# Optimization experiments

Measured on AMD Instinct MI355X. Metric: run time of the kernel, lower is better.

## Reference

```python
import jax, jax.numpy as jnp
import numpy as np

PHI_C = 0.9
ALPHA = 0.9
EPS = 1e-06
K_MAX = 100


def setup_inputs() -> dict:
    key = jax.random.key(0)
    k1, k2, k3 = jax.random.split(key, 3)
    B, D_IN, D_H, D_OUT = 16384, 1024, 4096, 1024
    x = jax.random.normal(k1, (B, D_IN), dtype=jnp.float32)
    W1 = jax.random.normal(k2, (D_IN, D_H), dtype=jnp.float32) * 0.02
    b1 = jnp.zeros((D_H,), dtype=jnp.float32)
    W2 = jax.random.normal(k3, (D_H, D_OUT), dtype=jnp.float32) * 0.02
    b2 = jnp.zeros((D_OUT,), dtype=jnp.float32)
    return {"x": x, "W1": W1, "b1": b1, "W2": W2, "b2": b2}


def _base_net(x, W1, b1, W2, b2):
    h = jax.nn.relu(x @ W1 + b1)
    return h @ W2 + b2  # [B, D_OUT]


def _fixed_point(out):
    # y_{k+1} = y_k + alpha * phi_c * tanh(out - y_k), with early exit when
    # max|y_{k+1} - y_k| < eps (the converging step IS applied, as in torch).
    y0 = jnp.zeros_like(out)

    def step(carry, _):
        y, done = carry
        y_next = y + ALPHA * PHI_C * jnp.tanh(out - y)
        converged = jnp.max(jnp.abs(y_next - y)) < EPS
        y_new = jnp.where(done, y, y_next)
        return (y_new, done | converged), None

    (y, _), _ = jax.lax.scan(step, (y0, jnp.array(False)), None, length=K_MAX)
    return y


def reference(x, W1, b1, W2, b2):
    out = _base_net(x, W1, b1, W2, b2)
    return _fixed_point(out)
```

## Files before the change

### kernel.cpp

```cpp
#include <hip/hip_runtime.h>
#include <hip/hip_bf16.h>
#include <stdint.h>


#define DEV __device__ __forceinline__

typedef short bf16x8 __attribute__((ext_vector_type(8)));
typedef float f32x4 __attribute__((ext_vector_type(4)));

typedef __attribute__((address_space(1))) const unsigned char* gptr1_t;
typedef __attribute__((address_space(3))) unsigned char* lptr3_t;

DEV void async_copy16(const void* g, void* l) {
  __builtin_amdgcn_global_load_lds((gptr1_t)g, (lptr3_t)l, 16, 0, 0);
}

DEV unsigned short f2bf(float f) {
  union { float f; unsigned u; } v; v.f = f;
  unsigned u = v.u + 0x7FFFu + ((v.u >> 16) & 1u);
  return (unsigned short)(u >> 16);
}

#define BAR()  __builtin_amdgcn_s_barrier()
#define VMW(n) asm volatile("s_waitcnt vmcnt(" #n ")" ::: "memory")


__global__ void cvt_f32_bf16(const float4* __restrict__ in,
                             ushort4* __restrict__ out, int n4) {
  int i = blockIdx.x * blockDim.x + threadIdx.x;
  if (i >= n4) return;
  float4 v = in[i];
  ushort4 o;
  o.x = f2bf(v.x); o.y = f2bf(v.y); o.z = f2bf(v.z); o.w = f2bf(v.w);
  out[i] = o;
}

__global__ void transpose_f32_bf16(const float* __restrict__ in,
                                   unsigned short* __restrict__ out,
                                   int R, int C) {
  __shared__ float tile[32][33];
  int c0 = blockIdx.x * 32, r0 = blockIdx.y * 32;
  int tx = threadIdx.x, ty = threadIdx.y;
#pragma unroll
  for (int i = 0; i < 32; i += 8)
    tile[ty + i][tx] = in[(long)(r0 + ty + i) * C + (c0 + tx)];
  __syncthreads();
#pragma unroll
  for (int i = 0; i < 32; i += 8)
    out[(long)(c0 + ty + i) * R + (r0 + tx)] = f2bf(tile[tx][ty + i]);
}


#define LDA(base, m, ks) \
  (*(const bf16x8*)((base) + abase + (m) * 2048 + (c0 ^ ((ks) << 6))))
#define LDB(base, n, ks) \
  (*(const bf16x8*)((base) + bbase + (n) * 2048 + (c0 ^ ((ks) << 6))))

#define RD_A(dst, base, m0_)                                   \
  _Pragma("unroll") for (int m_ = 0; m_ < 4; ++m_) {           \
    dst[m_][0] = LDA(base, (m0_) + m_, 0);                     \
    dst[m_][1] = LDA(base, (m0_) + m_, 1);                     \
  }
#define RD_B(dst, base, n0_)                                   \
  _Pragma("unroll") for (int n_ = 0; n_ < 2; ++n_) {           \
    dst[n_][0] = LDB(base, (n0_) + n_, 0);                     \
    dst[n_][1] = LDB(base, (n0_) + n_, 1);                     \
  }

#define QUAD(MB, NB, AF, BF)                                                \
  do {                                                                      \
    __builtin_amdgcn_s_setprio(1);                                          \
    _Pragma("unroll") for (int m_ = 0; m_ < 4; ++m_)                        \
    _Pragma("unroll") for (int n_ = 0; n_ < 2; ++n_) {                      \
      acc[(MB) + m_][(NB) + n_] = __builtin_amdgcn_mfma_f32_16x16x32_bf16(  \
          AF[m_][0], BF[n_][0], acc[(MB) + m_][(NB) + n_], 0, 0, 0);        \
      acc[(MB) + m_][(NB) + n_] = __builtin_amdgcn_mfma_f32_16x16x32_bf16(  \
          AF[m_][1], BF[n_][1], acc[(MB) + m_][(NB) + n_], 0, 0, 0);        \
    }                                                                       \
    __builtin_amdgcn_s_setprio(0);                                          \
  } while (0)

#define ST_A_LO(dstw, koff) { async_copy16(gA[0] + (koff), (dstw));          \
                              async_copy16(gA[2] + (koff), (dstw) + 16384); }
#define ST_A_HI(dstw, koff) { async_copy16(gA[1] + (koff), (dstw) + 8192);   \
                              async_copy16(gA[3] + (koff), (dstw) + 24576); }
#define ST_B_LO(dstw, koff) { async_copy16(gB[0] + (koff), (dstw));          \
                              async_copy16(gB[1] + (koff), (dstw) + 8192); }
#define ST_B_HI(dstw, koff) { async_copy16(gB[2] + (koff), (dstw) + 16384);  \
                              async_copy16(gB[3] + (koff), (dstw) + 24576); }

template <bool RELU_BF16>
__global__ __launch_bounds__(512, 2)
void gemm256(const unsigned short* __restrict__ A,
             const unsigned short* __restrict__ BT,
             const float* __restrict__ bias,
             void* __restrict__ Cout,
             int M, int N, int K, int nbn_shift) {
  extern __shared__ char lds[];
  const char* aE = lds;
  const char* aO = lds + 32768;
  const char* bE = lds + 65536;
  const char* bO = lds + 98304;

  const int tid = threadIdx.x;
  const int wave = tid >> 6, lane = tid & 63;
  const int wr = wave >> 2, wc = wave & 3;

  char* aEw = (char*)aE + wave * 1024;
  char* aOw = (char*)aO + wave * 1024;
  char* bEw = (char*)bE + wave * 1024;
  char* bOw = (char*)bO + wave * 1024;

  const int nwg = gridDim.x;
  const int wg = blockIdx.x;
  const int swz = (wg & 7) * (nwg >> 3) + (wg >> 3);
  const int bm = swz >> nbn_shift;
  const int bn = swz & ((1 << nbn_shift) - 1);
  const int m0 = bm << 8, n0 = bn << 8;

  const int srow = tid >> 3;
  const int sk = ((tid & 7) ^ (srow & 7)) << 3;
  const unsigned short* gA[4];
  const unsigned short* gB[4];
#pragma unroll
  for (int c = 0; c < 4; ++c) {
    gA[c] = A + (size_t)(m0 + c * 64 + srow) * K + sk;
    gB[c] = BT + (size_t)(n0 + c * 64 + srow) * K + sk;
  }

  const int lr = lane & 15, lg = lane >> 4;
  const int c0 = ((lg ^ (lr & 7)) << 4);
  const int abase = (wr * 128 + lr) * 128;
  const int bbase = (wc * 64 + lr) * 128;

  f32x4 acc[8][4] = {};
  bf16x8 af[4][2], b01[2][2], b23[2][2];

  ST_B_LO(bEw, 0);  ST_B_HI(bEw, 0);
  ST_A_LO(aEw, 0);  ST_A_HI(aEw, 0);
  ST_B_LO(bOw, 64); ST_B_HI(bOw, 64);
  VMW(4);
  BAR();

  const int NT = K >> 6;

  for (int it = 0; it < (NT - 2) / 2; ++it) {
    const int kE = (2 * it) << 6;
    RD_B(b01, bE, 0); RD_A(af, aE, 0); RD_B(b23, bE, 2);
    ST_A_LO(aOw, kE + 64); ST_A_HI(aOw, kE + 64);
    QUAD(0, 0, af, b01); QUAD(0, 2, af, b23);
    BAR();
    RD_A(af, aE, 4);
    ST_B_LO(bEw, kE + 128); ST_B_HI(bEw, kE + 128);
    QUAD(4, 2, af, b23); QUAD(4, 0, af, b01);
    VMW(4); BAR();
    RD_B(b01, bO, 0); RD_A(af, aO, 0); RD_B(b23, bO, 2);
    ST_A_LO(aEw, kE + 128); ST_A_HI(aEw, kE + 128);
    QUAD(0, 0, af, b01); QUAD(0, 2, af, b23);
    BAR();
    RD_A(af, aO, 4);
    ST_B_LO(bOw, kE + 192); ST_B_HI(bOw, kE + 192);
    QUAD(4, 2, af, b23); QUAD(4, 0, af, b01);
    VMW(4); BAR();
  }

  {
    const int kL = (NT - 1) << 6;
    RD_B(b01, bE, 0); RD_A(af, aE, 0); RD_B(b23, bE, 2);
    ST_A_LO(aOw, kL); ST_A_HI(aOw, kL);
    QUAD(0, 0, af, b01); QUAD(0, 2, af, b23);
    BAR();
    RD_A(af, aE, 4);
    QUAD(4, 2, af, b23); QUAD(4, 0, af, b01);
    VMW(0); BAR();
    RD_B(b01, bO, 0); RD_A(af, aO, 0); RD_B(b23, bO, 2);
    QUAD(0, 0, af, b01); QUAD(0, 2, af, b23);
    BAR();
    RD_A(af, aO, 4);
    QUAD(4, 2, af, b23); QUAD(4, 0, af, b01);
  }

  const int ccol = n0 + wc * 64;
  const int crow = m0 + wr * 128;
  float bv[4];
#pragma unroll
  for (int n = 0; n < 4; ++n) bv[n] = bias[ccol + n * 16 + lr];

  if (RELU_BF16) {
    unsigned short* O = (unsigned short*)Cout;
#pragma unroll
    for (int m = 0; m < 8; ++m)
#pragma unroll
      for (int j = 0; j < 4; ++j) {
        size_t r = (size_t)(crow + m * 16 + lg * 4 + j) * N;
#pragma unroll
        for (int n = 0; n < 4; ++n) {
          float v = acc[m][n][j] + bv[n];
          O[r + ccol + n * 16 + lr] = f2bf(fmaxf(v, 0.0f));
        }
      }
  } else {
    float* O = (float*)Cout;
#pragma unroll
    for (int m = 0; m < 8; ++m)
#pragma unroll
      for (int j = 0; j < 4; ++j) {
        size_t r = (size_t)(crow + m * 16 + lg * 4 + j) * N;
#pragma unroll
        for (int n = 0; n < 4; ++n)
          O[r + ccol + n * 16 + lr] = acc[m][n][j] + bv[n];
      }
  }
}


extern "C" void kernel_launch(void* const* d_in, const int* in_sizes, int n_in,
                              void* d_out, int out_size, void* d_ws,
                              size_t ws_size, hipStream_t stream) {
  const float* x  = (const float*)d_in[0];
  const float* W1 = (const float*)d_in[1];
  const float* b1 = (const float*)d_in[2];
  const float* W2 = (const float*)d_in[3];
  const float* b2 = (const float*)d_in[4];
  float* out = (float*)d_out;

  const int B = 16384, DIN = 1024, DH = 4096, DOUT = 1024;

  size_t need = (size_t)B * DIN * 2 + (size_t)DIN * DH * 2 +
                (size_t)DH * DOUT * 2 + (size_t)B * DH * 2;
  if (ws_size < need) return;

  char* ws = (char*)d_ws;
  unsigned short* xb  = (unsigned short*)ws;  ws += (size_t)B * DIN * 2;
  unsigned short* w1t = (unsigned short*)ws;  ws += (size_t)DIN * DH * 2;
  unsigned short* w2t = (unsigned short*)ws;  ws += (size_t)DH * DOUT * 2;
  unsigned short* h   = (unsigned short*)ws;

  hipFuncSetAttribute((const void*)gemm256<true>,
                      hipFuncAttributeMaxDynamicSharedMemorySize, 131072);
  hipFuncSetAttribute((const void*)gemm256<false>,
                      hipFuncAttributeMaxDynamicSharedMemorySize, 131072);

  int n4 = B * DIN / 4;
  cvt_f32_bf16<<<n4 / 256, 256, 0, stream>>>((const float4*)x, (ushort4*)xb, n4);
  transpose_f32_bf16<<<dim3(DH / 32, DIN / 32), dim3(32, 8), 0, stream>>>(W1, w1t, DIN, DH);
  transpose_f32_bf16<<<dim3(DOUT / 32, DH / 32), dim3(32, 8), 0, stream>>>(W2, w2t, DH, DOUT);

  gemm256<true><<<dim3((B / 256) * (DH / 256)), 512, 131072, stream>>>(
      xb, w1t, b1, h, B, DH, DIN, 4);
  gemm256<false><<<dim3((B / 256) * (DOUT / 256)), 512, 131072, stream>>>(
      h, w2t, b2, out, B, DOUT, DH, 2);
}
```

Baseline: 274.5 us.

## Use 4-wave 32x32x16 MFMA GEMM kernel for the first layer

Adds a new GEMM kernel with 256 threads (4 waves), each wave computing a 128x128 tile with 32x32x16 bf16 MFMAs and a double-buffered async global-to-LDS pipeline. It replaces the 8-wave 16x16 kernel for the first (ReLU, bf16 output) GEMM only. The aim is higher per-wave ILP and fewer LDS reads per FLOP. The trade-off is heavy register pressure from 256 accumulator floats per lane and only one workgroup per CU, which may hurt latency hiding.

```diff
diff --git a/kernel.cpp b/kernel.cpp
--- a/kernel.cpp
+++ b/kernel.cpp
@@ -7,6 +7,7 @@
 
 typedef short bf16x8 __attribute__((ext_vector_type(8)));
 typedef float f32x4 __attribute__((ext_vector_type(4)));
+typedef float f32x16 __attribute__((ext_vector_type(16)));
 
 typedef __attribute__((address_space(1))) const unsigned char* gptr1_t;
 typedef __attribute__((address_space(3))) unsigned char* lptr3_t;
@@ -21,8 +22,9 @@
   return (unsigned short)(u >> 16);
 }
 
-#define BAR()  __builtin_amdgcn_s_barrier()
-#define VMW(n) asm volatile("s_waitcnt vmcnt(" #n ")" ::: "memory")
+#define BAR()    __builtin_amdgcn_s_barrier()
+#define VMW(n)   asm volatile("s_waitcnt vmcnt(" #n ")" ::: "memory")
+#define SCHEDB() __builtin_amdgcn_sched_barrier(0)
 
 
 __global__ void cvt_f32_bf16(const float4* __restrict__ in,
@@ -48,6 +50,129 @@
 #pragma unroll
   for (int i = 0; i < 32; i += 8)
     out[(long)(c0 + ty + i) * R + (r0 + tx)] = f2bf(tile[tx][ty + i]);
+}
+
+
+#define ILDA(base, m, ks) \
+  (*(const bf16x8*)((base) + i_abase + (m) * 4096 + (i_c0 ^ ((ks) << 5))))
+#define ILDB(base, n, ks) \
+  (*(const bf16x8*)((base) + i_bbase + (n) * 4096 + (i_c0 ^ ((ks) << 5))))
+
+#define ICOMPUTE(aB, bB)                                                      \
+  _Pragma("unroll") for (int ks = 0; ks < 4; ++ks) {                          \
+    bf16x8 af[4], bfr[4];                                                     \
+    _Pragma("unroll") for (int i = 0; i < 4; ++i) {                           \
+      af[i] = ILDA(aB, i, ks);                                                \
+      bfr[i] = ILDB(bB, i, ks);                                               \
+    }                                                                         \
+    _Pragma("unroll") for (int m_ = 0; m_ < 4; ++m_)                          \
+    _Pragma("unroll") for (int n_ = 0; n_ < 4; ++n_)                          \
+      acc[m_][n_] = __builtin_amdgcn_mfma_f32_32x32x16_bf16(                  \
+          af[m_], bfr[n_], acc[m_][n_], 0, 0, 0);                             \
+  }
+
+#define ISTAGE(buf_, koff_)                                                   \
+  _Pragma("unroll") for (int j = 0; j < 8; ++j) {                             \
+    async_copy16(gAb + (size_t)j * 32 * K + (koff_),                          \
+                 ldsAw + (buf_) * 32768 + j * 4096);                          \
+    async_copy16(gBb + (size_t)j * 32 * K + (koff_),                          \
+                 ldsBw + (buf_) * 32768 + j * 4096);                          \
+  }
+
+template <bool RELU_BF16>
+__global__ __launch_bounds__(256, 1)
+void gemm_ilp4(const unsigned short* __restrict__ A,
+               const unsigned short* __restrict__ BT,
+               const float* __restrict__ bias,
+               void* __restrict__ Cout,
+               int M, int N, int K, int nbn_shift) {
+  extern __shared__ char lds[];
+  char* ldsA = lds;
+  char* ldsB = lds + 65536;
+
+  const int tid = threadIdx.x;
+  const int wave = tid >> 6, lane = tid & 63;
+  const int wr = wave >> 1, wc = wave & 1;
+
+  const int nwg = gridDim.x;
+  const int wg = blockIdx.x;
+  const int swz = (wg & 7) * (nwg >> 3) + (wg >> 3);
+  const int bm = swz >> nbn_shift;
+  const int bn = swz & ((1 << nbn_shift) - 1);
+  const int m0 = bm << 8, n0 = bn << 8;
+
+  const int srow = lane >> 3;
+  const int skb = (((lane & 7) ^ srow ^ wave) << 3);
+  const unsigned short* gAb = A + (size_t)(m0 + wave * 8 + srow) * K + skb;
+  const unsigned short* gBb = BT + (size_t)(n0 + wave * 8 + srow) * K + skb;
+  char* ldsAw = ldsA + wave * 1024;
+  char* ldsBw = ldsB + wave * 1024;
+
+  const int cl31 = lane & 31, lg2 = lane >> 5;
+  const int i_c0 = ((lg2 ^ (lane & 7) ^ ((lane >> 3) & 3)) << 4);
+  const int i_abase = (wr * 128 + cl31) * 128;
+  const int i_bbase = (wc * 128 + cl31) * 128;
+
+  f32x16 acc[4][4] = {};
+
+  ISTAGE(0, 0);
+  ISTAGE(1, 64);
+  VMW(16);
+  BAR();
+
+  const int NT = K >> 6;
+
+  for (int t = 0; t < NT - 2; ++t) {
+    const char* aB = ldsA + (t & 1) * 32768;
+    const char* bB = ldsB + (t & 1) * 32768;
+    ICOMPUTE(aB, bB);
+    BAR();
+    SCHEDB();
+    ISTAGE(t & 1, (t + 2) << 6);
+    VMW(16);
+    BAR();
+  }
+  ICOMPUTE(ldsA, ldsB);
+  BAR();
+  VMW(0);
+  BAR();
+  ICOMPUTE((ldsA + 32768), (ldsB + 32768));
+
+  const int ccol = n0 + wc * 128;
+  const int crow = m0 + wr * 128;
+  float bv[4];
+#pragma unroll
+  for (int n = 0; n < 4; ++n) bv[n] = bias[ccol + n * 32 + cl31];
+
+  if (RELU_BF16) {
+    unsigned short* O = (unsigned short*)Cout;
+#pragma unroll
+    for (int m = 0; m < 4; ++m)
+#pragma unroll
+      for (int rr = 0; rr < 4; ++rr)
+#pragma unroll
+        for (int q = 0; q < 4; ++q) {
+          size_t r = (size_t)(crow + m * 32 + lg2 * 4 + q + 8 * rr) * N;
+#pragma unroll
+          for (int n = 0; n < 4; ++n) {
+            float v = acc[m][n][rr * 4 + q] + bv[n];
+            O[r + ccol + n * 32 + cl31] = f2bf(fmaxf(v, 0.0f));
+          }
+        }
+  } else {
+    float* O = (float*)Cout;
+#pragma unroll
+    for (int m = 0; m < 4; ++m)
+#pragma unroll
+      for (int rr = 0; rr < 4; ++rr)
+#pragma unroll
+        for (int q = 0; q < 4; ++q) {
+          size_t r = (size_t)(crow + m * 32 + lg2 * 4 + q + 8 * rr) * N;
+#pragma unroll
+          for (int n = 0; n < 4; ++n)
+            O[r + ccol + n * 32 + cl31] = acc[m][n][rr * 4 + q] + bv[n];
+        }
+  }
 }
 
 
@@ -91,7 +216,7 @@
 
 template <bool RELU_BF16>
 __global__ __launch_bounds__(512, 2)
-void gemm256(const unsigned short* __restrict__ A,
+void gemm_w8(const unsigned short* __restrict__ A,
              const unsigned short* __restrict__ BT,
              const float* __restrict__ bias,
              void* __restrict__ Cout,
@@ -163,7 +288,6 @@
     QUAD(4, 2, af, b23); QUAD(4, 0, af, b01);
     VMW(4); BAR();
   }
-
   {
     const int kL = (NT - 1) << 6;
     RD_B(b01, bE, 0); RD_A(af, aE, 0); RD_B(b23, bE, 2);
@@ -236,9 +360,9 @@
   unsigned short* w2t = (unsigned short*)ws;  ws += (size_t)DH * DOUT * 2;
   unsigned short* h   = (unsigned short*)ws;
 
-  hipFuncSetAttribute((const void*)gemm256<true>,
+  hipFuncSetAttribute((const void*)gemm_ilp4<true>,
                       hipFuncAttributeMaxDynamicSharedMemorySize, 131072);
-  hipFuncSetAttribute((const void*)gemm256<false>,
+  hipFuncSetAttribute((const void*)gemm_w8<false>,
                       hipFuncAttributeMaxDynamicSharedMemorySize, 131072);
 
   int n4 = B * DIN / 4;
@@ -246,8 +370,8 @@
   transpose_f32_bf16<<<dim3(DH / 32, DIN / 32), dim3(32, 8), 0, stream>>>(W1, w1t, DIN, DH);
   transpose_f32_bf16<<<dim3(DOUT / 32, DH / 32), dim3(32, 8), 0, stream>>>(W2, w2t, DH, DOUT);
 
-  gemm256<true><<<dim3((B / 256) * (DH / 256)), 512, 131072, stream>>>(
+  gemm_ilp4<true><<<dim3((B / 256) * (DH / 256)), 256, 131072, stream>>>(
       xb, w1t, b1, h, B, DH, DIN, 4);
-  gemm256<false><<<dim3((B / 256) * (DOUT / 256)), 512, 131072, stream>>>(
+  gemm_w8<false><<<dim3((B / 256) * (DOUT / 256)), 512, 131072, stream>>>(
       h, w2t, b2, out, B, DOUT, DH, 2);
 }
```

Result: slower. 298.7 us (+8.9%).

## Make first GEMM persistent over four M tiles per workgroup

Applied to the files above, without the earlier changes.

Replaces the first GEMM launch of 1024 independent 256x256 tiles with 256 workgroups. Each walks four consecutive M tiles for a fixed N column, streaming K continuously across the tile boundary and flushing the bias+ReLU epilogue every 16 K-steps. This keeps the software pipeline full across tiles and avoids per-tile prologue/epilogue drain and launch overhead. The cost is a larger serial chain per workgroup with epilogue stores inside the main loop, and the B operand reloaded per tile since LDS holds no reuse.

```diff
diff --git a/kernel.cpp b/kernel.cpp
--- a/kernel.cpp
+++ b/kernel.cpp
@@ -89,9 +89,128 @@
 #define ST_B_HI(dstw, koff) { async_copy16(gB[2] + (koff), (dstw) + 16384);  \
                               async_copy16(gB[3] + (koff), (dstw) + 24576); }
 
+
+__global__ __launch_bounds__(512, 2)
+void gemm_w8p(const unsigned short* __restrict__ A,
+              const unsigned short* __restrict__ BT,
+              const float* __restrict__ bias,
+              unsigned short* __restrict__ O,
+              int K, int Ndim) {
+  extern __shared__ char lds[];
+  const char* aE = lds;
+  const char* aO = lds + 32768;
+  const char* bE = lds + 65536;
+  const char* bO = lds + 98304;
+
+  const int tid = threadIdx.x;
+  const int wave = tid >> 6, lane = tid & 63;
+  const int wr = wave >> 2, wc = wave & 3;
+
+  char* aEw = (char*)aE + wave * 1024;
+  char* aOw = (char*)aO + wave * 1024;
+  char* bEw = (char*)bE + wave * 1024;
+  char* bOw = (char*)bO + wave * 1024;
+
+  const int nwg = gridDim.x;
+  const int wg = blockIdx.x;
+  const int swz = (wg & 7) * (nwg >> 3) + (wg >> 3);
+  const int bn = swz & 15;
+  const int grp = swz >> 4;
+  const int n0 = bn << 8;
+  const int m0base = grp << 10;
+
+  const int srow = tid >> 3;
+  const int sk = ((tid & 7) ^ (srow & 7)) << 3;
+  const unsigned short* gA[4];
+  const unsigned short* gB[4];
+#pragma unroll
+  for (int c = 0; c < 4; ++c) {
+    gA[c] = A + (size_t)(m0base + c * 64 + srow) * K + sk;
+    gB[c] = BT + (size_t)(n0 + c * 64 + srow) * K + sk;
+  }
+
+  const int lr = lane & 15, lg = lane >> 4;
+  const int c0 = ((lg ^ (lr & 7)) << 4);
+  const int abase = (wr * 128 + lr) * 128;
+  const int bbase = (wc * 64 + lr) * 128;
+  const int ccol = n0 + wc * 64;
+
+  f32x4 acc[8][4] = {};
+  bf16x8 af[4][2], b01[2][2], b23[2][2];
+  float bv[4];
+#pragma unroll
+  for (int n = 0; n < 4; ++n) bv[n] = bias[ccol + n * 16 + lr];
+
+#define AOFF(g) ((size_t)((g) >> 4) * ((size_t)K << 8) + (size_t)(((g) & 15) << 6))
+#define BOFF(g) ((size_t)(((g) & 15) << 6))
+
+#define PEPI(j_)                                                              \
+  { const int crow = m0base + (j_) * 256 + wr * 128;                          \
+    _Pragma("unroll") for (int m = 0; m < 8; ++m)                             \
+    _Pragma("unroll") for (int jj = 0; jj < 4; ++jj) {                        \
+      size_t r = (size_t)(crow + m * 16 + lg * 4 + jj) * Ndim;                \
+      _Pragma("unroll") for (int n = 0; n < 4; ++n) {                         \
+        float v = acc[m][n][jj] + bv[n];                                      \
+        O[r + ccol + n * 16 + lr] = f2bf(fmaxf(v, 0.0f));                     \
+      } } }
+
+#define ZEROACC()                                                             \
+  _Pragma("unroll") for (int m = 0; m < 8; ++m)                               \
+  _Pragma("unroll") for (int n = 0; n < 4; ++n)                               \
+    acc[m][n] = (f32x4){0.f, 0.f, 0.f, 0.f};
+
+  ST_B_LO(bEw, 0);        ST_B_HI(bEw, 0);
+  ST_A_LO(aEw, 0);        ST_A_HI(aEw, 0);
+  ST_B_LO(bOw, BOFF(1));  ST_B_HI(bOw, BOFF(1));
+  VMW(4);
+  BAR();
+
+  for (int it = 0; it < 31; ++it) {
+    const int gE = 2 * it, gO = 2 * it + 1;
+    RD_B(b01, bE, 0); RD_A(af, aE, 0); RD_B(b23, bE, 2);
+    ST_A_LO(aOw, AOFF(gE + 1)); ST_A_HI(aOw, AOFF(gE + 1));
+    QUAD(0, 0, af, b01); QUAD(0, 2, af, b23);
+    BAR();
+    RD_A(af, aE, 4);
+    ST_B_LO(bEw, BOFF(gE + 2)); ST_B_HI(bEw, BOFF(gE + 2));
+    QUAD(4, 2, af, b23); QUAD(4, 0, af, b01);
+    VMW(4); BAR();
+    RD_B(b01, bO, 0); RD_A(af, aO, 0); RD_B(b23, bO, 2);
+    ST_A_LO(aEw, AOFF(gO + 1)); ST_A_HI(aEw, AOFF(gO + 1));
+    QUAD(0, 0, af, b01); QUAD(0, 2, af, b23);
+    BAR();
+    RD_A(af, aO, 4);
+    ST_B_LO(bOw, BOFF(gO + 2)); ST_B_HI(bOw, BOFF(gO + 2));
+    QUAD(4, 2, af, b23); QUAD(4, 0, af, b01);
+    VMW(4); BAR();
+    if ((it & 7) == 7) {
+      PEPI(gO >> 4);
+      ZEROACC();
+    }
+  }
+  RD_B(b01, bE, 0); RD_A(af, aE, 0); RD_B(b23, bE, 2);
+  ST_A_LO(aOw, AOFF(63)); ST_A_HI(aOw, AOFF(63));
+  QUAD(0, 0, af, b01); QUAD(0, 2, af, b23);
+  BAR();
+  RD_A(af, aE, 4);
+  QUAD(4, 2, af, b23); QUAD(4, 0, af, b01);
+  VMW(0); BAR();
+  RD_B(b01, bO, 0); RD_A(af, aO, 0); RD_B(b23, bO, 2);
+  QUAD(0, 0, af, b01); QUAD(0, 2, af, b23);
+  BAR();
+  RD_A(af, aO, 4);
+  QUAD(4, 2, af, b23); QUAD(4, 0, af, b01);
+  PEPI(3);
+#undef PEPI
+#undef ZEROACC
+#undef AOFF
+#undef BOFF
+}
+
+
 template <bool RELU_BF16>
 __global__ __launch_bounds__(512, 2)
-void gemm256(const unsigned short* __restrict__ A,
+void gemm_w8(const unsigned short* __restrict__ A,
              const unsigned short* __restrict__ BT,
              const float* __restrict__ bias,
              void* __restrict__ Cout,
@@ -163,7 +282,6 @@
     QUAD(4, 2, af, b23); QUAD(4, 0, af, b01);
     VMW(4); BAR();
   }
-
   {
     const int kL = (NT - 1) << 6;
     RD_B(b01, bE, 0); RD_A(af, aE, 0); RD_B(b23, bE, 2);
@@ -236,9 +354,9 @@
   unsigned short* w2t = (unsigned short*)ws;  ws += (size_t)DH * DOUT * 2;
   unsigned short* h   = (unsigned short*)ws;
 
-  hipFuncSetAttribute((const void*)gemm256<true>,
+  hipFuncSetAttribute((const void*)gemm_w8p,
                       hipFuncAttributeMaxDynamicSharedMemorySize, 131072);
-  hipFuncSetAttribute((const void*)gemm256<false>,
+  hipFuncSetAttribute((const void*)gemm_w8<false>,
                       hipFuncAttributeMaxDynamicSharedMemorySize, 131072);
 
   int n4 = B * DIN / 4;
@@ -246,8 +364,7 @@
   transpose_f32_bf16<<<dim3(DH / 32, DIN / 32), dim3(32, 8), 0, stream>>>(W1, w1t, DIN, DH);
   transpose_f32_bf16<<<dim3(DOUT / 32, DH / 32), dim3(32, 8), 0, stream>>>(W2, w2t, DH, DOUT);
 
-  gemm256<true><<<dim3((B / 256) * (DH / 256)), 512, 131072, stream>>>(
-      xb, w1t, b1, h, B, DH, DIN, 4);
-  gemm256<false><<<dim3((B / 256) * (DOUT / 256)), 512, 131072, stream>>>(
+  gemm_w8p<<<dim3(256), 512, 131072, stream>>>(xb, w1t, b1, h, DIN, DH);
+  gemm_w8<false><<<dim3((B / 256) * (DOUT / 256)), 512, 131072, stream>>>(
       h, w2t, b2, out, B, DOUT, DH, 2);
 }
```

Result: no change. 272.7 us (-0.6%).
